# Kernel optimization log

Measured on AMD Instinct MI355X. Metric: run time of the kernel, lower is better.

## Reference

```python
import jax, jax.numpy as jnp
import numpy as np

EPS = 1e-12  # matches torch F.normalize eps


def _l2_normalize(x):
    # F.normalize(x, p=2, dim=1): divide by clamped norm
    norm = jnp.sqrt(jnp.sum(x * x, axis=1, keepdims=True))
    return x / jnp.maximum(norm, EPS)


def setup_inputs() -> dict:
    key = jax.random.key(0)
    k1, k2, k3 = jax.random.split(key, 3)
    N, D, P, C = 16384, 768, 2048, 1000
    h = jax.random.normal(k1, (N, D), dtype=jnp.float32)
    prototypes = jax.random.normal(k2, (P, D), dtype=jnp.float32) * 0.1
    prototype_class = jax.random.normal(k3, (P, C), dtype=jnp.float32)
    temperature = jnp.float32(1.0)
    return {"h": h, "prototypes": prototypes,
            "prototype_class": prototype_class, "temperature": temperature}


def reference(h, prototypes, prototype_class, temperature):
    h_norm = _l2_normalize(h)                      # [N, D]
    p_norm = _l2_normalize(prototypes)             # [P, D]
    # cdist (p=2): sqrt(||a||^2 + ||b||^2 - 2 a.b), clamped at 0
    h_sq = jnp.sum(h_norm * h_norm, axis=1, keepdims=True)   # [N, 1]
    p_sq = jnp.sum(p_norm * p_norm, axis=1)                  # [P]
    dots = jnp.einsum('nd,pd->np', h_norm, p_norm)           # [N, P]
    dist_sq = jnp.maximum(h_sq + p_sq[None, :] - 2.0 * dots, 0.0)
    distances = jnp.sqrt(dist_sq)                            # [N, P]
    tau = jax.nn.softplus(temperature)
    activations = jnp.exp(-tau * distances)                  # [N, P]
    class_logits = jnp.matmul(activations, prototype_class)  # [N, C]
    return class_logits
```

## Files before the change

### kernel.cpp

```cpp
#include <hip/hip_runtime.h>
#include <hip/hip_bf16.h>
#include <math.h>

typedef unsigned short ushort_t;
typedef unsigned char uchar_t;
typedef unsigned int uint_t;
typedef __attribute__((ext_vector_type(8))) short bf16x8;
typedef __attribute__((ext_vector_type(4))) float f32x4;
typedef __attribute__((ext_vector_type(2))) long longx2;

#define AS1 __attribute__((address_space(1)))
#define AS3 __attribute__((address_space(3)))

__device__ __forceinline__ void gld_lds16(const void* g, void* l) {
  __builtin_amdgcn_global_load_lds((const AS1 void*)g, (AS3 void*)l, 16, 0, 0);
}

__device__ __forceinline__ ushort_t f32_to_bf16_bits(float v) {
  __hip_bfloat16 b = __float2bfloat16(v);
  return *(ushort_t*)&b;
}

__device__ __forceinline__ uint_t pack_fp8x4(float4 v, float sc) {
  int r = __builtin_amdgcn_cvt_pk_fp8_f32(v.x * sc, v.y * sc, 0, false);
  r = __builtin_amdgcn_cvt_pk_fp8_f32(v.z * sc, v.w * sc, r, true);
  return (uint_t)r;
}


__global__ __launch_bounds__(256) void prep(const float4* __restrict__ h,
                                            uchar_t* __restrict__ h8, int rowsH,
                                            const float4* __restrict__ p,
                                            uchar_t* __restrict__ p8, int rowsP,
                                            const float* __restrict__ pc,
                                            ushort_t* __restrict__ pcT,
                                            int P, int C, int normBlocks) {
  __shared__ float tile[32][33];
  if ((int)blockIdx.x < normBlocks) {
    int r = (blockIdx.x * 256 + threadIdx.x) >> 6;
    const int lane = threadIdx.x & 63;
    const float4* xr;
    uchar_t* o8;
    if (r < rowsH) {
      xr = h + (size_t)r * 192;
      o8 = h8;
    } else {
      r -= rowsH;
      if (r >= rowsP) return;
      xr = p + (size_t)r * 192;
      o8 = p8;
    }
    float4 v0 = xr[lane];
    float4 v1 = xr[lane + 64];
    float4 v2 = xr[lane + 128];
    float ss = v0.x * v0.x + v0.y * v0.y + v0.z * v0.z + v0.w * v0.w
             + v1.x * v1.x + v1.y * v1.y + v1.z * v1.z + v1.w * v1.w
             + v2.x * v2.x + v2.y * v2.y + v2.z * v2.z + v2.w * v2.w;
#pragma unroll
    for (int off = 32; off > 0; off >>= 1) ss += __shfl_xor(ss, off, 64);
    const float sc = 4.0f / fmaxf(sqrtf(ss), 1e-12f);
    const int rb = r >> 4, rl = r & 15;
    const int key4 = (rl >> 1) & 3;
    const int u = (lane & 7) >> 1;
    const int ksub = (lane & 15) >> 3;
    const int cphys = ((u ^ key4) << 4) + (ksub << 3) + ((lane & 1) << 2);
    const int ktb = lane >> 4;
    uchar_t* rowbase = o8 + (size_t)rb * 12 * 1024 + rl * 64 + cphys;
    *(uint_t*)(rowbase + (size_t)(ktb) * 1024)     = pack_fp8x4(v0, sc);
    *(uint_t*)(rowbase + (size_t)(4 + ktb) * 1024) = pack_fp8x4(v1, sc);
    *(uint_t*)(rowbase + (size_t)(8 + ktb) * 1024) = pack_fp8x4(v2, sc);
  } else {
    const int b = blockIdx.x - normBlocks;
    const int nkb = P / 32;
    const int bk = b % nkb, bc = b / nkb;
    const int k0 = bk * 32, c0 = bc * 32;
    const int tx = threadIdx.x & 31, ty = threadIdx.x >> 5;
#pragma unroll
    for (int rr = 0; rr < 4; ++rr) {
      const int c = c0 + tx;
      tile[ty + rr * 8][tx] = (c < C) ? pc[(size_t)(k0 + ty + rr * 8) * C + c] : 0.f;
    }
    __syncthreads();
    const int c2 = tx >> 3, off = tx & 7;
#pragma unroll
    for (int rr = 0; rr < 4; ++rr) {
      const int row = c0 + ty + rr * 8;
      const int rb = row >> 4, rl = row & 15;
      const int key4 = (rl >> 1) & 3;
      size_t us = (((size_t)rb * nkb + bk) * 16 + rl) * 32 + ((c2 ^ key4) << 3) + off;
      pcT[us] = f32_to_bf16_bits(tile[tx][ty + rr * 8]);
    }
  }
}

#define BARRIER() do { asm volatile("" ::: "memory"); __builtin_amdgcn_s_barrier(); \
                       asm volatile("" ::: "memory"); } while (0)
#define LGKM0()   asm volatile("s_waitcnt lgkmcnt(0)" ::: "memory")
#define VM6()     asm volatile("s_waitcnt vmcnt(6)" ::: "memory")
#define VM3()     asm volatile("s_waitcnt vmcnt(3)" ::: "memory")
#define VM0()     asm volatile("s_waitcnt vmcnt(0)" ::: "memory")
#define PRIO1()   __builtin_amdgcn_s_setprio(1)
#define PRIO0()   __builtin_amdgcn_s_setprio(0)
#define MM(a, b, c)  __builtin_amdgcn_mfma_f32_16x16x32_bf16(a, b, c, 0, 0, 0)
#define MM8(a, b, c) __builtin_amdgcn_mfma_f32_16x16x32_fp8_fp8(a, b, c, 0, 0, 0)

#define PH_MFMA8(I0, I1, A0_, A1_)                                                            \
  acc[I0][0] = MM8(A0_[0], bb0[0], acc[I0][0]); acc[I0][1] = MM8(A0_[0], bb1[0], acc[I0][1]); \
  acc[I0][2] = MM8(A0_[0], bb2[0], acc[I0][2]); acc[I0][3] = MM8(A0_[0], bb3[0], acc[I0][3]); \
  acc[I1][0] = MM8(A1_[0], bb0[0], acc[I1][0]); acc[I1][1] = MM8(A1_[0], bb1[0], acc[I1][1]); \
  acc[I1][2] = MM8(A1_[0], bb2[0], acc[I1][2]); acc[I1][3] = MM8(A1_[0], bb3[0], acc[I1][3]); \
  acc[I0][0] = MM8(A0_[1], bb0[1], acc[I0][0]); acc[I0][1] = MM8(A0_[1], bb1[1], acc[I0][1]); \
  acc[I0][2] = MM8(A0_[1], bb2[1], acc[I0][2]); acc[I0][3] = MM8(A0_[1], bb3[1], acc[I0][3]); \
  acc[I1][0] = MM8(A1_[1], bb0[1], acc[I1][0]); acc[I1][1] = MM8(A1_[1], bb1[1], acc[I1][1]); \
  acc[I1][2] = MM8(A1_[1], bb2[1], acc[I1][2]); acc[I1][3] = MM8(A1_[1], bb3[1], acc[I1][3])

__launch_bounds__(512, 2)
__global__ void gemm1_fp8_8ph(const uchar_t* __restrict__ A, const uchar_t* __restrict__ B,
                              ushort_t* __restrict__ act, const float* __restrict__ tptr,
                              int nKt, int actKT, int gx, int gxlog2) {
  __shared__ __align__(16) uchar_t sm1[65536];
  const int tid = threadIdx.x, lane = tid & 63, wave = tid >> 6;
  const int wm = wave >> 2, wn = wave & 3;
  const int lid = blockIdx.x, xcd = lid & 7, q = lid >> 3;
  const int tb = q & (gx - 1), sb = ((q >> gxlog2) << 3) | xcd;

  f32x4 acc[8][4];
#pragma unroll
  for (int i = 0; i < 8; ++i)
#pragma unroll
    for (int j = 0; j < 4; ++j) acc[i][j] = (f32x4){0.f, 0.f, 0.f, 0.f};

  const int m2 = (wave & 4) ? wave + 4 : wave;
  const int m3 = m2 + 4;
  const uchar_t* Apl = A + (((size_t)(sb * 16) * nKt) << 10) + lane * 16;
  const uchar_t* Bpl = B + (((size_t)(tb * 16) * nKt) << 10) + lane * 16;

  const int fr = lane & 15, g = lane >> 4;
  const int rdoff = fr * 64 + ((g ^ ((fr >> 1) & 3)) << 4);
  const int wm8 = wm * 8, wn4 = wn * 4;

#define F_STA(m_, T_, bo_) gld_lds16(Apl + (((size_t)(m_) * nKt + (T_)) << 10), \
                                     sm1 + (bo_) + ((m_) << 10))
#define F_STB(m_, T_, bo_) gld_lds16(Bpl + (((size_t)(m_) * nKt + (T_)) << 10), \
                                     sm1 + (bo_) + 16384 + ((m_) << 10))
#define F_DSA(i_) (*(const longx2*)(sm1 + bufoff + ((wm8 + (i_)) << 10) + rdoff))
#define F_DSB(j_) (*(const longx2*)(sm1 + bufoff + 16384 + ((wn4 + (j_)) << 10) + rdoff))

  F_STB(wave, 0, 0); F_STB(wave + 8, 0, 0); F_STA(m2, 0, 0); F_STA(m3, 0, 0);
  F_STB(wave, 1, 32768); F_STB(wave + 8, 1, 32768); F_STA(m2, 1, 32768);
  VM3(); BARRIER();

  for (int kt = 0; kt < nKt; ++kt) {
    const int bufoff = (kt & 1) << 15;
    const int nbo = ((kt + 1) & 1) << 15;
    longx2 bb0 = F_DSB(0), bb1 = F_DSB(1), bb2 = F_DSB(2), bb3 = F_DSB(3);
    longx2 a0v = F_DSA(0), a1v = F_DSA(1);
    if (kt + 1 < nKt) { F_STA(m3, kt + 1, nbo); }
    BARRIER(); LGKM0();
    PRIO1();
    PH_MFMA8(0, 1, a0v, a1v);
    PRIO0();
    BARRIER();
    {
      longx2 a2v = F_DSA(2), a3v = F_DSA(3);
      if (kt + 2 < nKt) { F_STB(wave, kt + 2, bufoff); }
      BARRIER(); LGKM0();
      PRIO1();
      PH_MFMA8(2, 3, a2v, a3v);
      PRIO0();
      BARRIER();
    }
    {
      longx2 a4v = F_DSA(4), a5v = F_DSA(5);
      if (kt + 2 < nKt) { F_STB(wave + 8, kt + 2, bufoff); }
      BARRIER(); LGKM0();
      PRIO1();
      PH_MFMA8(4, 5, a4v, a5v);
      PRIO0();
      BARRIER();
    }
    {
      longx2 a6v = F_DSA(6), a7v = F_DSA(7);
      if (kt + 2 < nKt) { F_STA(m2, kt + 2, bufoff); }
      BARRIER(); LGKM0();
      PRIO1();
      PH_MFMA8(6, 7, a6v, a7v);
      PRIO0();
      if (kt + 2 < nKt) { VM3(); } else { VM0(); }
      BARRIER();
    }
  }

  float tmp = *tptr;
  const float tau = log1pf(expf(tmp));
  const int crow = g * 4;
  const int rowB = sb * 256 + wm * 128, colB = tb * 256 + wn * 64;
#pragma unroll
  for (int i = 0; i < 8; ++i)
#pragma unroll
    for (int j = 0; j < 4; ++j) {
      const int col = colB + j * 16 + fr;
      const size_t ktile = col >> 5;
      const int c2 = (col >> 3) & 3, co = col & 7;
#pragma unroll
      for (int rr = 0; rr < 4; ++rr) {
        const int row = rowB + i * 16 + crow + rr;
        const int rb = row >> 4, rl = row & 15;
        const int key4 = (rl >> 1) & 3;
        float d2 = fmaxf(2.0f - acc[i][j][rr] * 0.125f, 0.0f);
        float a = __expf(-tau * sqrtf(d2));
        act[(((size_t)rb * actKT + ktile) * 16 + rl) * 32 + ((c2 ^ key4) << 3) + co] =
            f32_to_bf16_bits(a);
      }
    }
}


#define PHASE_MFMA(I0, I1, A00, A01, A10, A11)                                   \
  acc[I0][0] = MM(A00, b00, acc[I0][0]); acc[I0][1] = MM(A00, b10, acc[I0][1]);  \
  acc[I0][2] = MM(A00, b20, acc[I0][2]); acc[I0][3] = MM(A00, b30, acc[I0][3]);  \
  acc[I1][0] = MM(A10, b00, acc[I1][0]); acc[I1][1] = MM(A10, b10, acc[I1][1]);  \
  acc[I1][2] = MM(A10, b20, acc[I1][2]); acc[I1][3] = MM(A10, b30, acc[I1][3]);  \
  acc[I0][0] = MM(A01, b01, acc[I0][0]); acc[I0][1] = MM(A01, b11, acc[I0][1]);  \
  acc[I0][2] = MM(A01, b21, acc[I0][2]); acc[I0][3] = MM(A01, b31, acc[I0][3]);  \
  acc[I1][0] = MM(A11, b01, acc[I1][0]); acc[I1][1] = MM(A11, b11, acc[I1][1]);  \
  acc[I1][2] = MM(A11, b21, acc[I1][2]); acc[I1][3] = MM(A11, b31, acc[I1][3])

__launch_bounds__(512, 2)
__global__ void gemm2_bf16_8ph(const ushort_t* __restrict__ A,
                               const ushort_t* __restrict__ B,
                               float* __restrict__ out, int ldc, int ncols,
                               int nKt) {
  __shared__ __align__(16) uchar_t sm[131072];
  const int tid = threadIdx.x, lane = tid & 63, wave = tid >> 6;
  const int wm = wave >> 2, wn = wave & 3;
  const int lid = blockIdx.x, xcd = lid & 7, q = lid >> 3;
  const int tb = q & 3, sb = ((q >> 2) << 3) | xcd;

  f32x4 acc[8][4];
#pragma unroll
  for (int i = 0; i < 8; ++i)
#pragma unroll
    for (int j = 0; j < 4; ++j) acc[i][j] = (f32x4){0.f, 0.f, 0.f, 0.f};

  const int lw = wave & 1, rw = wave >> 1;
  const uchar_t* Apl = (const uchar_t*)A + ((size_t)(sb * 16) << 16) + (lw << 10) + lane * 16;
  const uchar_t* Bpl = (const uchar_t*)B + ((size_t)(tb * 16) << 16) + (lw << 10) + lane * 16;

  const int fr = lane & 15, g = lane >> 4;
  const int rdoff = fr * 64 + ((g ^ ((fr >> 1) & 3)) << 4);
  const int wm8 = wm * 8, wn4 = wn * 4;

#define STA(r_, T_, bo_) gld_lds16(Apl + (((size_t)(r_) << 16) + ((size_t)(T_) << 11)), \
                                   sm + (bo_) + ((((r_) << 1) + lw) << 10))
#define STB(r_, T_, bo_) gld_lds16(Bpl + (((size_t)(r_) << 16) + ((size_t)(T_) << 11)), \
                                   sm + (bo_) + 32768 + ((((r_) << 1) + lw) << 10))
#define DSA(i_, l_) (*(const bf16x8*)(sm + bufoff + (((wm8 + (i_)) * 2 + (l_)) << 10) + rdoff))
#define DSB(j_, l_) (*(const bf16x8*)(sm + bufoff + 32768 + (((wn4 + (j_)) * 2 + (l_)) << 10) + rdoff))

  STB(rw, 0, 0); STB(rw + 4, 0, 0); STB(rw + 8, 0, 0); STB(rw + 12, 0, 0);
  STA(rw, 0, 0); STA(rw + 8, 0, 0); STA(rw + 4, 0, 0); STA(rw + 12, 0, 0);
  STB(rw, 1, 65536); STB(rw + 4, 1, 65536); STB(rw + 8, 1, 65536); STB(rw + 12, 1, 65536);
  STA(rw, 1, 65536); STA(rw + 8, 1, 65536);
  VM6(); BARRIER();

  for (int kt = 0; kt < nKt; ++kt) {
    const int bufoff = (kt & 1) << 16;
    const int nbo = ((kt + 1) & 1) << 16;
    bf16x8 b00 = DSB(0, 0), b01 = DSB(0, 1), b10 = DSB(1, 0), b11 = DSB(1, 1);
    bf16x8 b20 = DSB(2, 0), b21 = DSB(2, 1), b30 = DSB(3, 0), b31 = DSB(3, 1);
    bf16x8 a00 = DSA(0, 0), a01 = DSA(0, 1), a10 = DSA(1, 0), a11 = DSA(1, 1);
    if (kt + 1 < nKt) { STA(rw + 4, kt + 1, nbo); STA(rw + 12, kt + 1, nbo); }
    BARRIER(); LGKM0();
    PRIO1();
    PHASE_MFMA(0, 1, a00, a01, a10, a11);
    PRIO0();
    BARRIER();
    {
      bf16x8 a20 = DSA(2, 0), a21 = DSA(2, 1), a30 = DSA(3, 0), a31 = DSA(3, 1);
      if (kt + 2 < nKt) { STB(rw, kt + 2, bufoff); STB(rw + 4, kt + 2, bufoff); }
      BARRIER(); LGKM0();
      PRIO1();
      PHASE_MFMA(2, 3, a20, a21, a30, a31);
      PRIO0();
      BARRIER();
    }
    {
      bf16x8 a40 = DSA(4, 0), a41 = DSA(4, 1), a50 = DSA(5, 0), a51 = DSA(5, 1);
      if (kt + 2 < nKt) { STB(rw + 8, kt + 2, bufoff); STB(rw + 12, kt + 2, bufoff); }
      BARRIER(); LGKM0();
      PRIO1();
      PHASE_MFMA(4, 5, a40, a41, a50, a51);
      PRIO0();
      BARRIER();
    }
    {
      bf16x8 a60 = DSA(6, 0), a61 = DSA(6, 1), a70 = DSA(7, 0), a71 = DSA(7, 1);
      if (kt + 2 < nKt) { STA(rw, kt + 2, bufoff); STA(rw + 8, kt + 2, bufoff); }
      BARRIER(); LGKM0();
      PRIO1();
      PHASE_MFMA(6, 7, a60, a61, a70, a71);
      PRIO0();
      if (kt + 2 < nKt) { VM6(); } else { VM0(); }
      BARRIER();
    }
  }

  const int crow = g * 4;
  const int rowB = sb * 256 + wm * 128, colB = tb * 256 + wn * 64;
#pragma unroll
  for (int i = 0; i < 8; ++i)
#pragma unroll
    for (int j = 0; j < 4; ++j) {
      const int col = colB + j * 16 + fr;
      if (col < ncols) {
#pragma unroll
        for (int rr = 0; rr < 4; ++rr)
          out[(size_t)(rowB + i * 16 + crow + rr) * ldc + col] = acc[i][j][rr];
      }
    }
}

extern "C" void kernel_launch(void* const* d_in, const int* in_sizes, int n_in,
                              void* d_out, int out_size, void* d_ws, size_t ws_size,
                              hipStream_t stream) {
  const float* h    = (const float*)d_in[0];
  const float* prot = (const float*)d_in[1];
  const float* pc   = (const float*)d_in[2];
  const float* temp = (const float*)d_in[3];
  float* out = (float*)d_out;

  const int D = 768;
  const int N = in_sizes[0] / D;
  const int P = in_sizes[1] / D;
  const int C = in_sizes[2] / P;
  const int CP = (C + 127) & ~127;

  char* ws = (char*)d_ws;
  size_t off = 0;
  uchar_t* h8   = (uchar_t*)(ws + off); off += (size_t)N * D;
  uchar_t* p8   = (uchar_t*)(ws + off); off += (size_t)P * D;
  ushort_t* pcT = (ushort_t*)(ws + off); off += (size_t)CP * P * 2;
  ushort_t* act = (ushort_t*)(ws + off); off += (size_t)N * P * 2;
  (void)ws_size;

  const int normBlocks = (N + P) / 4;
  const int transBlocks = (P / 32) * (CP / 32);
  prep<<<normBlocks + transBlocks, 256, 0, stream>>>(
      (const float4*)h, h8, N, (const float4*)prot, p8, P,
      pc, pcT, P, C, normBlocks);

  {
    const int GX = P / 256, GY = N / 256;
    gemm1_fp8_8ph<<<GX * GY, 512, 0, stream>>>(h8, p8, act, temp, D / 64, P / 32, GX, 3);
  }
  {
    const int GX = CP / 256, GY = N / 256;
    gemm2_bf16_8ph<<<GX * GY, 512, 0, stream>>>(act, pcT, out, C, C, P / 64);
  }
}
```

Baseline: 236.2 us.

## Software-pipeline LDS fragment reads one phase ahead of MFMAs in both GEMMs

```diff
diff --git a/kernel.cpp b/kernel.cpp
--- a/kernel.cpp
+++ b/kernel.cpp
@@ -96,28 +96,30 @@
 #define BARRIER() do { asm volatile("" ::: "memory"); __builtin_amdgcn_s_barrier(); \
                        asm volatile("" ::: "memory"); } while (0)
 #define LGKM0()   asm volatile("s_waitcnt lgkmcnt(0)" ::: "memory")
-#define VM6()     asm volatile("s_waitcnt vmcnt(6)" ::: "memory")
-#define VM3()     asm volatile("s_waitcnt vmcnt(3)" ::: "memory")
+#define VM8()     asm volatile("s_waitcnt vmcnt(8)" ::: "memory")
+#define VM4()     asm volatile("s_waitcnt vmcnt(4)" ::: "memory")
+#define VM2()     asm volatile("s_waitcnt vmcnt(2)" ::: "memory")
 #define VM0()     asm volatile("s_waitcnt vmcnt(0)" ::: "memory")
 #define PRIO1()   __builtin_amdgcn_s_setprio(1)
 #define PRIO0()   __builtin_amdgcn_s_setprio(0)
+#define SB0()     __builtin_amdgcn_sched_barrier(0)
 #define MM(a, b, c)  __builtin_amdgcn_mfma_f32_16x16x32_bf16(a, b, c, 0, 0, 0)
 #define MM8(a, b, c) __builtin_amdgcn_mfma_f32_16x16x32_fp8_fp8(a, b, c, 0, 0, 0)
 
-#define PH_MFMA8(I0, I1, A0_, A1_)                                                            \
-  acc[I0][0] = MM8(A0_[0], bb0[0], acc[I0][0]); acc[I0][1] = MM8(A0_[0], bb1[0], acc[I0][1]); \
-  acc[I0][2] = MM8(A0_[0], bb2[0], acc[I0][2]); acc[I0][3] = MM8(A0_[0], bb3[0], acc[I0][3]); \
-  acc[I1][0] = MM8(A1_[0], bb0[0], acc[I1][0]); acc[I1][1] = MM8(A1_[0], bb1[0], acc[I1][1]); \
-  acc[I1][2] = MM8(A1_[0], bb2[0], acc[I1][2]); acc[I1][3] = MM8(A1_[0], bb3[0], acc[I1][3]); \
-  acc[I0][0] = MM8(A0_[1], bb0[1], acc[I0][0]); acc[I0][1] = MM8(A0_[1], bb1[1], acc[I0][1]); \
-  acc[I0][2] = MM8(A0_[1], bb2[1], acc[I0][2]); acc[I0][3] = MM8(A0_[1], bb3[1], acc[I0][3]); \
-  acc[I1][0] = MM8(A1_[1], bb0[1], acc[I1][0]); acc[I1][1] = MM8(A1_[1], bb1[1], acc[I1][1]); \
-  acc[I1][2] = MM8(A1_[1], bb2[1], acc[I1][2]); acc[I1][3] = MM8(A1_[1], bb3[1], acc[I1][3])
+#define MFMA16_8(I0, I1, A0_, A1_)                                                              \
+  acc[I0][0] = MM8(A0_[0], bC[0][0], acc[I0][0]); acc[I0][1] = MM8(A0_[0], bC[1][0], acc[I0][1]); \
+  acc[I0][2] = MM8(A0_[0], bC[2][0], acc[I0][2]); acc[I0][3] = MM8(A0_[0], bC[3][0], acc[I0][3]); \
+  acc[I1][0] = MM8(A1_[0], bC[0][0], acc[I1][0]); acc[I1][1] = MM8(A1_[0], bC[1][0], acc[I1][1]); \
+  acc[I1][2] = MM8(A1_[0], bC[2][0], acc[I1][2]); acc[I1][3] = MM8(A1_[0], bC[3][0], acc[I1][3]); \
+  acc[I0][0] = MM8(A0_[1], bC[0][1], acc[I0][0]); acc[I0][1] = MM8(A0_[1], bC[1][1], acc[I0][1]); \
+  acc[I0][2] = MM8(A0_[1], bC[2][1], acc[I0][2]); acc[I0][3] = MM8(A0_[1], bC[3][1], acc[I0][3]); \
+  acc[I1][0] = MM8(A1_[1], bC[0][1], acc[I1][0]); acc[I1][1] = MM8(A1_[1], bC[1][1], acc[I1][1]); \
+  acc[I1][2] = MM8(A1_[1], bC[2][1], acc[I1][2]); acc[I1][3] = MM8(A1_[1], bC[3][1], acc[I1][3])
 
 __launch_bounds__(512, 2)
-__global__ void gemm1_fp8_8ph(const uchar_t* __restrict__ A, const uchar_t* __restrict__ B,
-                              ushort_t* __restrict__ act, const float* __restrict__ tptr,
-                              int nKt, int actKT, int gx, int gxlog2) {
+__global__ void gemm1_fp8_la(const uchar_t* __restrict__ A, const uchar_t* __restrict__ B,
+                             ushort_t* __restrict__ act, const float* __restrict__ tptr,
+                             int nKt, int actKT, int gx, int gxlog2) {
   __shared__ __align__(16) uchar_t sm1[65536];
   const int tid = threadIdx.x, lane = tid & 63, wave = tid >> 6;
   const int wm = wave >> 2, wn = wave & 3;
@@ -143,52 +145,42 @@
                                      sm1 + (bo_) + ((m_) << 10))
 #define F_STB(m_, T_, bo_) gld_lds16(Bpl + (((size_t)(m_) * nKt + (T_)) << 10), \
                                      sm1 + (bo_) + 16384 + ((m_) << 10))
-#define F_DSA(i_) (*(const longx2*)(sm1 + bufoff + ((wm8 + (i_)) << 10) + rdoff))
-#define F_DSB(j_) (*(const longx2*)(sm1 + bufoff + 16384 + ((wn4 + (j_)) << 10) + rdoff))
+#define F_DSA_AT(bo_, i_) (*(const longx2*)(sm1 + (bo_) + ((wm8 + (i_)) << 10) + rdoff))
+#define F_DSB_AT(bo_, j_) (*(const longx2*)(sm1 + (bo_) + 16384 + ((wn4 + (j_)) << 10) + rdoff))
 
   F_STB(wave, 0, 0); F_STB(wave + 8, 0, 0); F_STA(m2, 0, 0); F_STA(m3, 0, 0);
-  F_STB(wave, 1, 32768); F_STB(wave + 8, 1, 32768); F_STA(m2, 1, 32768);
-  VM3(); BARRIER();
-
+  F_STB(wave, 1, 32768); F_STB(wave + 8, 1, 32768); F_STA(m2, 1, 32768); F_STA(m3, 1, 32768);
+  VM4(); BARRIER();
+
+  longx2 bC[4], aP[2], bN[4], aN[2];
+  bC[0] = F_DSB_AT(0, 0); bC[1] = F_DSB_AT(0, 1); bC[2] = F_DSB_AT(0, 2); bC[3] = F_DSB_AT(0, 3);
+  aP[0] = F_DSA_AT(0, 0); aP[1] = F_DSA_AT(0, 1);
+  LGKM0(); BARRIER();
+
+#pragma unroll 2
   for (int kt = 0; kt < nKt; ++kt) {
     const int bufoff = (kt & 1) << 15;
     const int nbo = ((kt + 1) & 1) << 15;
-    longx2 bb0 = F_DSB(0), bb1 = F_DSB(1), bb2 = F_DSB(2), bb3 = F_DSB(3);
-    longx2 a0v = F_DSA(0), a1v = F_DSA(1);
-    if (kt + 1 < nKt) { F_STA(m3, kt + 1, nbo); }
-    BARRIER(); LGKM0();
-    PRIO1();
-    PH_MFMA8(0, 1, a0v, a1v);
-    PRIO0();
-    BARRIER();
-    {
-      longx2 a2v = F_DSA(2), a3v = F_DSA(3);
-      if (kt + 2 < nKt) { F_STB(wave, kt + 2, bufoff); }
-      BARRIER(); LGKM0();
-      PRIO1();
-      PH_MFMA8(2, 3, a2v, a3v);
-      PRIO0();
-      BARRIER();
-    }
-    {
-      longx2 a4v = F_DSA(4), a5v = F_DSA(5);
-      if (kt + 2 < nKt) { F_STB(wave + 8, kt + 2, bufoff); }
-      BARRIER(); LGKM0();
-      PRIO1();
-      PH_MFMA8(4, 5, a4v, a5v);
-      PRIO0();
-      BARRIER();
-    }
-    {
-      longx2 a6v = F_DSA(6), a7v = F_DSA(7);
-      if (kt + 2 < nKt) { F_STA(m2, kt + 2, bufoff); }
-      BARRIER(); LGKM0();
-      PRIO1();
-      PH_MFMA8(6, 7, a6v, a7v);
-      PRIO0();
-      if (kt + 2 < nKt) { VM3(); } else { VM0(); }
-      BARRIER();
-    }
+    longx2 aQ[2];
+    aQ[0] = F_DSA_AT(bufoff, 2); aQ[1] = F_DSA_AT(bufoff, 3);
+    if (kt + 2 < nKt) F_STB(wave, kt + 2, bufoff);
+    SB0(); PRIO1(); MFMA16_8(0, 1, aP[0], aP[1]); PRIO0(); LGKM0(); SB0(); BARRIER();
+    aP[0] = F_DSA_AT(bufoff, 4); aP[1] = F_DSA_AT(bufoff, 5);
+    if (kt + 2 < nKt) F_STB(wave + 8, kt + 2, bufoff);
+    SB0(); PRIO1(); MFMA16_8(2, 3, aQ[0], aQ[1]); PRIO0(); LGKM0(); SB0(); BARRIER();
+    if (kt + 1 < nKt) { if (kt + 2 < nKt) { VM2(); } else { VM0(); } }
+    aQ[0] = F_DSA_AT(bufoff, 6); aQ[1] = F_DSA_AT(bufoff, 7);
+    if (kt + 1 < nKt) { bN[0] = F_DSB_AT(nbo, 0); bN[1] = F_DSB_AT(nbo, 1); }
+    if (kt + 2 < nKt) F_STA(m2, kt + 2, bufoff);
+    SB0(); PRIO1(); MFMA16_8(4, 5, aP[0], aP[1]); PRIO0(); LGKM0(); SB0(); BARRIER();
+    if (kt + 1 < nKt) {
+      bN[2] = F_DSB_AT(nbo, 2); bN[3] = F_DSB_AT(nbo, 3);
+      aN[0] = F_DSA_AT(nbo, 0); aN[1] = F_DSA_AT(nbo, 1);
+    }
+    if (kt + 2 < nKt) F_STA(m3, kt + 2, bufoff);
+    SB0(); PRIO1(); MFMA16_8(6, 7, aQ[0], aQ[1]); PRIO0(); LGKM0(); SB0(); BARRIER();
+    bC[0] = bN[0]; bC[1] = bN[1]; bC[2] = bN[2]; bC[3] = bN[3];
+    aP[0] = aN[0]; aP[1] = aN[1];
   }
 
   float tmp = *tptr;
@@ -215,22 +207,21 @@
     }
 }
 
-
-#define PHASE_MFMA(I0, I1, A00, A01, A10, A11)                                   \
-  acc[I0][0] = MM(A00, b00, acc[I0][0]); acc[I0][1] = MM(A00, b10, acc[I0][1]);  \
-  acc[I0][2] = MM(A00, b20, acc[I0][2]); acc[I0][3] = MM(A00, b30, acc[I0][3]);  \
-  acc[I1][0] = MM(A10, b00, acc[I1][0]); acc[I1][1] = MM(A10, b10, acc[I1][1]);  \
-  acc[I1][2] = MM(A10, b20, acc[I1][2]); acc[I1][3] = MM(A10, b30, acc[I1][3]);  \
-  acc[I0][0] = MM(A01, b01, acc[I0][0]); acc[I0][1] = MM(A01, b11, acc[I0][1]);  \
-  acc[I0][2] = MM(A01, b21, acc[I0][2]); acc[I0][3] = MM(A01, b31, acc[I0][3]);  \
-  acc[I1][0] = MM(A11, b01, acc[I1][0]); acc[I1][1] = MM(A11, b11, acc[I1][1]);  \
-  acc[I1][2] = MM(A11, b21, acc[I1][2]); acc[I1][3] = MM(A11, b31, acc[I1][3])
+#define MFMA16(I0, I1, AP, BC)                                                          \
+  acc[I0][0] = MM(AP[0], BC[0], acc[I0][0]); acc[I0][1] = MM(AP[0], BC[2], acc[I0][1]); \
+  acc[I0][2] = MM(AP[0], BC[4], acc[I0][2]); acc[I0][3] = MM(AP[0], BC[6], acc[I0][3]); \
+  acc[I1][0] = MM(AP[2], BC[0], acc[I1][0]); acc[I1][1] = MM(AP[2], BC[2], acc[I1][1]); \
+  acc[I1][2] = MM(AP[2], BC[4], acc[I1][2]); acc[I1][3] = MM(AP[2], BC[6], acc[I1][3]); \
+  acc[I0][0] = MM(AP[1], BC[1], acc[I0][0]); acc[I0][1] = MM(AP[1], BC[3], acc[I0][1]); \
+  acc[I0][2] = MM(AP[1], BC[5], acc[I0][2]); acc[I0][3] = MM(AP[1], BC[7], acc[I0][3]); \
+  acc[I1][0] = MM(AP[3], BC[1], acc[I1][0]); acc[I1][1] = MM(AP[3], BC[3], acc[I1][1]); \
+  acc[I1][2] = MM(AP[3], BC[5], acc[I1][2]); acc[I1][3] = MM(AP[3], BC[7], acc[I1][3])
 
 __launch_bounds__(512, 2)
-__global__ void gemm2_bf16_8ph(const ushort_t* __restrict__ A,
-                               const ushort_t* __restrict__ B,
-                               float* __restrict__ out, int ldc, int ncols,
-                               int nKt) {
+__global__ void gemm2_bf16_la(const ushort_t* __restrict__ A,
+                              const ushort_t* __restrict__ B,
+                              float* __restrict__ out, int ldc, int ncols,
+                              int nKt) {
   __shared__ __align__(16) uchar_t sm[131072];
   const int tid = threadIdx.x, lane = tid & 63, wave = tid >> 6;
   const int wm = wave >> 2, wn = wave & 3;
@@ -255,55 +246,55 @@
                                    sm + (bo_) + ((((r_) << 1) + lw) << 10))
 #define STB(r_, T_, bo_) gld_lds16(Bpl + (((size_t)(r_) << 16) + ((size_t)(T_) << 11)), \
                                    sm + (bo_) + 32768 + ((((r_) << 1) + lw) << 10))
-#define DSA(i_, l_) (*(const bf16x8*)(sm + bufoff + (((wm8 + (i_)) * 2 + (l_)) << 10) + rdoff))
-#define DSB(j_, l_) (*(const bf16x8*)(sm + bufoff + 32768 + (((wn4 + (j_)) * 2 + (l_)) << 10) + rdoff))
+#define DSA_AT(bo_, i_, l_) (*(const bf16x8*)(sm + (bo_) + (((wm8 + (i_)) * 2 + (l_)) << 10) + rdoff))
+#define DSB_AT(bo_, j_, l_) (*(const bf16x8*)(sm + (bo_) + 32768 + (((wn4 + (j_)) * 2 + (l_)) << 10) + rdoff))
 
   STB(rw, 0, 0); STB(rw + 4, 0, 0); STB(rw + 8, 0, 0); STB(rw + 12, 0, 0);
   STA(rw, 0, 0); STA(rw + 8, 0, 0); STA(rw + 4, 0, 0); STA(rw + 12, 0, 0);
   STB(rw, 1, 65536); STB(rw + 4, 1, 65536); STB(rw + 8, 1, 65536); STB(rw + 12, 1, 65536);
-  STA(rw, 1, 65536); STA(rw + 8, 1, 65536);
-  VM6(); BARRIER();
-
+  STA(rw, 1, 65536); STA(rw + 8, 1, 65536); STA(rw + 4, 1, 65536); STA(rw + 12, 1, 65536);
+  VM8(); BARRIER();
+
+  bf16x8 bC[8], aP[4], bN[8], aN[4];
+  bC[0] = DSB_AT(0, 0, 0); bC[1] = DSB_AT(0, 0, 1); bC[2] = DSB_AT(0, 1, 0); bC[3] = DSB_AT(0, 1, 1);
+  bC[4] = DSB_AT(0, 2, 0); bC[5] = DSB_AT(0, 2, 1); bC[6] = DSB_AT(0, 3, 0); bC[7] = DSB_AT(0, 3, 1);
+  aP[0] = DSA_AT(0, 0, 0); aP[1] = DSA_AT(0, 0, 1); aP[2] = DSA_AT(0, 1, 0); aP[3] = DSA_AT(0, 1, 1);
+  LGKM0(); BARRIER();
+
+#pragma unroll 2
   for (int kt = 0; kt < nKt; ++kt) {
     const int bufoff = (kt & 1) << 16;
     const int nbo = ((kt + 1) & 1) << 16;
-    bf16x8 b00 = DSB(0, 0), b01 = DSB(0, 1), b10 = DSB(1, 0), b11 = DSB(1, 1);
-    bf16x8 b20 = DSB(2, 0), b21 = DSB(2, 1), b30 = DSB(3, 0), b31 = DSB(3, 1);
-    bf16x8 a00 = DSA(0, 0), a01 = DSA(0, 1), a10 = DSA(1, 0), a11 = DSA(1, 1);
-    if (kt + 1 < nKt) { STA(rw + 4, kt + 1, nbo); STA(rw + 12, kt + 1, nbo); }
-    BARRIER(); LGKM0();
-    PRIO1();
-    PHASE_MFMA(0, 1, a00, a01, a10, a11);
-    PRIO0();
-    BARRIER();
-    {
-      bf16x8 a20 = DSA(2, 0), a21 = DSA(2, 1), a30 = DSA(3, 0), a31 = DSA(3, 1);
-      if (kt + 2 < nKt) { STB(rw, kt + 2, bufoff); STB(rw + 4, kt + 2, bufoff); }
-      BARRIER(); LGKM0();
-      PRIO1();
-      PHASE_MFMA(2, 3, a20, a21, a30, a31);
-      PRIO0();
-      BARRIER();
-    }
-    {
-      bf16x8 a40 = DSA(4, 0), a41 = DSA(4, 1), a50 = DSA(5, 0), a51 = DSA(5, 1);
-      if (kt + 2 < nKt) { STB(rw + 8, kt + 2, bufoff); STB(rw + 12, kt + 2, bufoff); }
-      BARRIER(); LGKM0();
-      PRIO1();
-      PHASE_MFMA(4, 5, a40, a41, a50, a51);
-      PRIO0();
-      BARRIER();
-    }
-    {
-      bf16x8 a60 = DSA(6, 0), a61 = DSA(6, 1), a70 = DSA(7, 0), a71 = DSA(7, 1);
-      if (kt + 2 < nKt) { STA(rw, kt + 2, bufoff); STA(rw + 8, kt + 2, bufoff); }
-      BARRIER(); LGKM0();
-      PRIO1();
-      PHASE_MFMA(6, 7, a60, a61, a70, a71);
-      PRIO0();
-      if (kt + 2 < nKt) { VM6(); } else { VM0(); }
-      BARRIER();
-    }
+    bf16x8 aQ[4];
+    aQ[0] = DSA_AT(bufoff, 2, 0); aQ[1] = DSA_AT(bufoff, 2, 1);
+    aQ[2] = DSA_AT(bufoff, 3, 0); aQ[3] = DSA_AT(bufoff, 3, 1);
+    if (kt + 2 < nKt) { STB(rw, kt + 2, bufoff); STB(rw + 4, kt + 2, bufoff); }
+    SB0(); PRIO1(); MFMA16(0, 1, aP, bC); PRIO0(); LGKM0(); SB0(); BARRIER();
+    aP[0] = DSA_AT(bufoff, 4, 0); aP[1] = DSA_AT(bufoff, 4, 1);
+    aP[2] = DSA_AT(bufoff, 5, 0); aP[3] = DSA_AT(bufoff, 5, 1);
+    if (kt + 2 < nKt) { STB(rw + 8, kt + 2, bufoff); STB(rw + 12, kt + 2, bufoff); }
+    SB0(); PRIO1(); MFMA16(2, 3, aQ, bC); PRIO0(); LGKM0(); SB0(); BARRIER();
+    if (kt + 1 < nKt) { if (kt + 2 < nKt) { VM4(); } else { VM0(); } }
+    aQ[0] = DSA_AT(bufoff, 6, 0); aQ[1] = DSA_AT(bufoff, 6, 1);
+    aQ[2] = DSA_AT(bufoff, 7, 0); aQ[3] = DSA_AT(bufoff, 7, 1);
+    if (kt + 1 < nKt) {
+      bN[0] = DSB_AT(nbo, 0, 0); bN[1] = DSB_AT(nbo, 0, 1);
+      bN[2] = DSB_AT(nbo, 1, 0); bN[3] = DSB_AT(nbo, 1, 1);
+    }
+    if (kt + 2 < nKt) { STA(rw, kt + 2, bufoff); STA(rw + 8, kt + 2, bufoff); }
+    SB0(); PRIO1(); MFMA16(4, 5, aP, bC); PRIO0(); LGKM0(); SB0(); BARRIER();
+    if (kt + 1 < nKt) {
+      bN[4] = DSB_AT(nbo, 2, 0); bN[5] = DSB_AT(nbo, 2, 1);
+      bN[6] = DSB_AT(nbo, 3, 0); bN[7] = DSB_AT(nbo, 3, 1);
+      aN[0] = DSA_AT(nbo, 0, 0); aN[1] = DSA_AT(nbo, 0, 1);
+      aN[2] = DSA_AT(nbo, 1, 0); aN[3] = DSA_AT(nbo, 1, 1);
+    }
+    if (kt + 2 < nKt) { STA(rw + 4, kt + 2, bufoff); STA(rw + 12, kt + 2, bufoff); }
+    SB0(); PRIO1(); MFMA16(6, 7, aQ, bC); PRIO0(); LGKM0(); SB0(); BARRIER();
+#pragma unroll
+    for (int k = 0; k < 8; ++k) bC[k] = bN[k];
+#pragma unroll
+    for (int k = 0; k < 4; ++k) aP[k] = aN[k];
   }
 
   const int crow = g * 4;
@@ -352,10 +343,10 @@
 
   {
     const int GX = P / 256, GY = N / 256;
-    gemm1_fp8_8ph<<<GX * GY, 512, 0, stream>>>(h8, p8, act, temp, D / 64, P / 32, GX, 3);
+    gemm1_fp8_la<<<GX * GY, 512, 0, stream>>>(h8, p8, act, temp, D / 64, P / 32, GX, 3);
   }
   {
     const int GX = CP / 256, GY = N / 256;
-    gemm2_bf16_8ph<<<GX * GY, 512, 0, stream>>>(act, pcT, out, C, C, P / 64);
-  }
-}
+    gemm2_bf16_la<<<GX * GY, 512, 0, stream>>>(act, pcT, out, C, C, P / 64);
+  }
+}
```

Result: slower. 263.1 us (+11.4%).
